# Kernel optimization log

Hardware: AMD Instinct MI355X
Metric: run time of the kernel (lower is better)

Reference implementation:

```python
import jax, jax.numpy as jnp
import numpy as np

N = 1024      # nodes per graph sample
B = 64        # batch size
D_IN = 64     # input feature dim
UNITS = 64    # num_units
K = 2         # max_diffusion_step
NUM_MATRICES = 2 * K + 1


def _random_walk_T(adj):
    # calculate_random_walk_matrix(adj).T == (D^-1 A)^T
    d = adj.sum(axis=1)
    d_inv = jnp.where(d > 0, 1.0 / d, 0.0)
    return (d_inv[:, None] * adj).T


def setup_inputs() -> dict:
    key = jax.random.key(0)
    k1, k2, k3, k4, k5, k6 = jax.random.split(key, 6)
    inputs = jax.random.normal(k1, (B * N, D_IN), dtype=jnp.float32)
    hx = jax.random.normal(k2, (B * N, UNITS), dtype=jnp.float32)
    # sparse-ish weighted adjacency -> random walk Laplacians (transposed) as in Gconv
    adj = jax.random.uniform(k3, (N, N), dtype=jnp.float32)
    adj = adj * (adj > 0.97)
    L0 = _random_walk_T(adj)
    L1 = _random_walk_T(adj.T)
    fan_in = (D_IN + UNITS) * NUM_MATRICES  # 640
    # xavier-normal-ish init
    W1 = jax.random.normal(k4, (fan_in, 2 * UNITS), dtype=jnp.float32) * np.sqrt(2.0 / (fan_in + 2 * UNITS))
    b1 = jnp.zeros((2 * UNITS,), dtype=jnp.float32)
    W2 = jax.random.normal(k5, (fan_in, UNITS), dtype=jnp.float32) * np.sqrt(2.0 / (fan_in + UNITS))
    b2 = jnp.zeros((UNITS,), dtype=jnp.float32)
    return {"inputs": inputs, "hx": hx, "L0": L0, "L1": L1,
            "W1": W1, "b1": b1, "W2": W2, "b2": b2, "batch_size": B}


def _gconv(x_flat, L0, L1, W, b, batch_size):
    # x_flat: [B*N, F]. Chebyshev-style diffusion with two directed random-walk
    # operators (block-diagonal sparse.mm in the original == per-sample matmul).
    n = L0.shape[0]
    f = x_flat.shape[-1]
    x = x_flat.reshape(batch_size, n, f)            # [B, N, F]
    x0a, x0b = x, x
    x1a = jnp.einsum('mn,bnf->bmf', L0, x0a)
    x1b = jnp.einsum('mn,bnf->bmf', L1, x0b)
    outs = [x, x1a, x1b]
    for _ in range(2, K + 1):
        x2a = 2.0 * jnp.einsum('mn,bnf->bmf', L0, x1a) - x0a
        x2b = 2.0 * jnp.einsum('mn,bnf->bmf', L1, x1b) - x0b
        outs += [x2a, x2b]
        x1a, x0a = x2a, x1a
        x1b, x0b = x2b, x1b
    xk = jnp.stack(outs, axis=-1)                   # [B, N, F, num_matrices]
    xk = xk.reshape(batch_size * n, f * NUM_MATRICES)
    return xk @ W + b


def reference(inputs, hx, L0, L1, W1, b1, W2, b2, batch_size):
    # DCGRUCell.forward
    xin = jnp.concatenate([inputs, hx], axis=-1)          # [B*N, D_IN+UNITS]
    value = jax.nn.sigmoid(_gconv(xin, L0, L1, W1, b1, batch_size))
    r, u = jnp.split(value, 2, axis=-1)                   # each [B*N, UNITS]
    xin2 = jnp.concatenate([inputs, r * hx], axis=-1)
    c = jnp.tanh(_gconv(xin2, L0, L1, W2, b2, batch_size))
    new_state = u * hx + (1.0 - u) * c
    return new_state
```

## Files before the change

kernel.cpp:

```cpp
#include <hip/hip_runtime.h>
#include <math.h>

#define N_NODES 1024
#define BATCH   64
#define F_IN    128
#define UNITS   64
#define NUM_M   5
#define CAP     192
#define NT1     640
#define NT2     320
#define DSTR    12

typedef __attribute__((ext_vector_type(8))) short short8v;
typedef __attribute__((ext_vector_type(4))) float f32x4;

__device__ __forceinline__ unsigned short bf16_rne(float x) {
    unsigned u = __float_as_uint(x);
    return (unsigned short)((u + 0x7FFFu + ((u >> 16) & 1u)) >> 16);
}

__global__ void degree_count(const float* __restrict__ L, int* __restrict__ dcnt) {
    int row  = blockIdx.x * 4 + (threadIdx.x >> 6);
    int lane = threadIdx.x & 63;
    const float* Lr = L + (size_t)row * N_NODES;
    int c = 0;
    for (int seg = lane; seg < N_NODES; seg += 64) c += (Lr[seg] != 0.0f);
    #pragma unroll
    for (int o = 1; o < 64; o <<= 1) c += __shfl_xor(c, o);
    if (lane == 0) dcnt[row] = c;
}

__global__ void sort_perm(const int* __restrict__ dcnt, int* __restrict__ perm) {
    __shared__ int hist[CAP + 1];
    __shared__ int offs[CAP + 1];
    int tid = threadIdx.x;
    for (int i = tid; i <= CAP; i += 256) hist[i] = 0;
    __syncthreads();
    for (int r = tid; r < N_NODES; r += 256) {
        int c = dcnt[r]; if (c > CAP) c = CAP;
        atomicAdd(&hist[c], 1);
    }
    __syncthreads();
    if (tid == 0) {
        int s = 0;
        for (int c = CAP; c >= 0; --c) { offs[c] = s; s += hist[c]; }
    }
    __syncthreads();
    for (int r = tid; r < N_NODES; r += 256) {
        int c = dcnt[r]; if (c > CAP) c = CAP;
        int pos = atomicAdd(&offs[c], 1);
        perm[pos] = r;
    }
}

__global__ void ell_build(const float* __restrict__ L, const int* __restrict__ perm,
                          int* __restrict__ scnt, float2* __restrict__ ell) {
    int p    = blockIdx.x * 4 + (threadIdx.x >> 6);
    int lane = threadIdx.x & 63;
    int row  = perm[p];
    const float* Lr = L + (size_t)row * N_NODES;
    int base = 0;
    for (int seg = 0; seg < N_NODES; seg += 64) {
        float v = Lr[seg + lane];
        bool nz = (v != 0.0f);
        unsigned long long bal = __ballot(nz);
        int off = __popcll(bal & ((1ull << lane) - 1ull));
        if (nz) {
            int idx = base + off;
            if (idx < CAP) ell[(size_t)idx * N_NODES + p] =
                               make_float2(__int_as_float(seg + lane), v);
        }
        base += __popcll(bal);
    }
    if (base > CAP) base = CAP;
    for (int idx = base + lane; idx < CAP; idx += 64)
        ell[(size_t)idx * N_NODES + p] = make_float2(__int_as_float(0), 0.0f);
    if (lane == 0) scnt[p] = (base + 3) & ~3;
}

__global__ void wprep_frag(const float* __restrict__ W, unsigned short* __restrict__ Wh,
                           unsigned short* __restrict__ Wl, int nout, int ntot) {
    int idx = blockIdx.x * blockDim.x + threadIdx.x;
    if (idx >= F_IN * ntot) return;
    int jg = idx % ntot, k = idx / ntot;
    int m = jg / nout, j = jg % nout;
    const float* Wk = W + (size_t)(k * NUM_M) * nout;
    float v;
    if (m == 0)      v = Wk[0 * nout + j] - Wk[3 * nout + j] - Wk[4 * nout + j];
    else if (m == 3) v = 2.0f * Wk[3 * nout + j];
    else if (m == 4) v = 2.0f * Wk[4 * nout + j];
    else             v = Wk[(size_t)m * nout + j];
    unsigned short h = bf16_rne(v);
    float hf = __uint_as_float((unsigned)h << 16);
    unsigned short lo = bf16_rne(v - hf);
    size_t fi = ((((size_t)(jg >> 4) * 4 + (k >> 5)) * 64) + ((k >> 3) & 3) * 16 + (jg & 15)) * 8 + (k & 7);
    Wh[fi] = h; Wl[fi] = lo;
}

template <int NCG, int RMUL>
__global__ __launch_bounds__(128, 3) void gemm_proj(
        const float* __restrict__ inp, const float* __restrict__ hx,
        const float* __restrict__ rh,
        const unsigned short* __restrict__ Wh, const unsigned short* __restrict__ Wl,
        float* __restrict__ P, int nrows, int row0) {
    const int tid = threadIdx.x;
    const int lane = tid & 63, w = tid >> 6;
    const int l15 = lane & 15, l4 = lane >> 4;
    const int nbase = blockIdx.x * 64 + w * 32;

    short8v ah[2][4], al[2][4];
    #pragma unroll
    for (int i = 0; i < 2; ++i)
        #pragma unroll
        for (int s = 0; s < 4; ++s) {
            int row_l = nbase + i * 16 + l15;
            int kg8 = s * 4 + l4;
            size_t g = (size_t)(row0 + row_l);
            float x[8];
            if (kg8 < 8) {
                *(float4*)&x[0] = *(const float4*)(inp + g * 64 + kg8 * 8);
                *(float4*)&x[4] = *(const float4*)(inp + g * 64 + kg8 * 8 + 4);
            } else if (RMUL) {
                const float* rp = rh + ((size_t)(kg8 - 8) * nrows + row_l) * 8;
                *(float4*)&x[0] = *(const float4*)(rp);
                *(float4*)&x[4] = *(const float4*)(rp + 4);
            } else {
                *(float4*)&x[0] = *(const float4*)(hx + g * 64 + (kg8 - 8) * 8);
                *(float4*)&x[4] = *(const float4*)(hx + g * 64 + (kg8 - 8) * 8 + 4);
            }
            #pragma unroll
            for (int e = 0; e < 8; ++e) {
                unsigned short h = bf16_rne(x[e]);
                ah[i][s][e] = (short)h;
                al[i][s][e] = (short)bf16_rne(x[e] - __uint_as_float((unsigned)h << 16));
            }
        }

    const int trow = l4 >> 1, toff = (l4 & 1) * 4;
    #pragma unroll 1
    for (int cg = 0; cg < NCG; ++cg) {
        f32x4 acc[2];
        acc[0] = (f32x4){0.f, 0.f, 0.f, 0.f};
        acc[1] = (f32x4){0.f, 0.f, 0.f, 0.f};
        #pragma unroll
        for (int s = 0; s < 4; ++s) {
            size_t o = (((size_t)cg * 4 + s) * 64 + lane) * 8;
            short8v bh = *(const short8v*)(Wh + o);
            short8v bl = *(const short8v*)(Wl + o);
            #pragma unroll
            for (int i = 0; i < 2; ++i) {
                acc[i] = __builtin_amdgcn_mfma_f32_16x16x32_bf16(bh, al[i][s], acc[i], 0, 0, 0);
                acc[i] = __builtin_amdgcn_mfma_f32_16x16x32_bf16(bl, ah[i][s], acc[i], 0, 0, 0);
                acc[i] = __builtin_amdgcn_mfma_f32_16x16x32_bf16(bh, ah[i][s], acc[i], 0, 0, 0);
            }
        }
        #pragma unroll
        for (int i = 0; i < 2; ++i) {
            float4 v = make_float4(acc[i][0], acc[i][1], acc[i][2], acc[i][3]);
            *(float4*)(P + ((size_t)(cg * 2 + trow) * nrows + (nbase + i * 16 + l15)) * 8 + toff) = v;
        }
    }
}

__device__ __forceinline__ void gather2x4(
        const float2* __restrict__ ell, const float* __restrict__ ldsX,
        int tid, int nmax, float4 acc[4][2]) {
    #pragma unroll
    for (int k = 0; k < 4; ++k) {
        acc[k][0] = make_float4(0.f, 0.f, 0.f, 0.f);
        acc[k][1] = make_float4(0.f, 0.f, 0.f, 0.f);
    }
    for (int j = 0; j < nmax; j += 2) {
        const float* e0 = (const float*)(ell + (size_t)j * N_NODES) + (size_t)tid * 8;
        const float* e1 = (const float*)(ell + (size_t)(j + 1) * N_NODES) + (size_t)tid * 8;
        float4 q00 = *(const float4*)e0, q01 = *(const float4*)(e0 + 4);
        float4 q10 = *(const float4*)e1, q11 = *(const float4*)(e1 + 4);
        float cf[2][4], wv[2][4];
        cf[0][0] = q00.x; wv[0][0] = q00.y; cf[0][1] = q00.z; wv[0][1] = q00.w;
        cf[0][2] = q01.x; wv[0][2] = q01.y; cf[0][3] = q01.z; wv[0][3] = q01.w;
        cf[1][0] = q10.x; wv[1][0] = q10.y; cf[1][1] = q10.z; wv[1][1] = q10.w;
        cf[1][2] = q11.x; wv[1][2] = q11.y; cf[1][3] = q11.z; wv[1][3] = q11.w;
        #pragma unroll
        for (int u = 0; u < 2; ++u)
            #pragma unroll
            for (int k = 0; k < 4; ++k) {
                int c = __float_as_int(cf[u][k]);
                float w = wv[u][k];
                const float* xp = ldsX + (size_t)c * DSTR;
                float4 x0 = *(const float4*)xp;
                float4 x1 = *(const float4*)(xp + 4);
                acc[k][0].x += w * x0.x; acc[k][0].y += w * x0.y;
                acc[k][0].z += w * x0.z; acc[k][0].w += w * x0.w;
                acc[k][1].x += w * x1.x; acc[k][1].y += w * x1.y;
                acc[k][1].z += w * x1.z; acc[k][1].w += w * x1.w;
            }
    }
}

__global__ __launch_bounds__(256, 3) void diffuse2(
        const int* __restrict__ scnt0, const float2* __restrict__ ell0, const int* __restrict__ perm0,
        const int* __restrict__ scnt1, const float2* __restrict__ ell1, const int* __restrict__ perm1,
        float* __restrict__ P, size_t sl, int nrows) {
    __shared__ float ldsX[N_NODES * DSTR];
    const int tid = threadIdx.x;
    const int z = blockIdx.z;
    const int*    scnt = z ? scnt1 : scnt0;
    const float2* ell  = z ? ell1  : ell0;
    const int*    perm = z ? perm1 : perm0;
    const float*  src  = P + (size_t)(z ? 4 : 3) * sl;
    float*        dst  = P + (size_t)(z ? 2 : 1) * sl;
    const size_t base = ((size_t)blockIdx.x * nrows + (size_t)blockIdx.y * N_NODES) * 8;

    for (int v = tid; v < 2048; v += 256) {
        float4 d = *(const float4*)(src + base + v * 4);
        *(float4*)(ldsX + (v >> 1) * DSTR + (v & 1) * 4) = d;
    }
    int4 pr = *(const int4*)(perm + tid * 4);
    int4 cn = *(const int4*)(scnt + tid * 4);
    int orow[4] = {pr.x, pr.y, pr.z, pr.w};
    int nn4 = max(max(cn.x, cn.y), max(cn.z, cn.w));
    __syncthreads();

    float4 T[4][2];
    gather2x4(ell, ldsX, tid, nn4, T);
    __syncthreads();
    #pragma unroll
    for (int k = 0; k < 4; ++k) {
        const float* ap = dst + base + (size_t)orow[k] * 8;
        float4 a0 = *(const float4*)ap, a1 = *(const float4*)(ap + 4);
        T[k][0].x += a0.x; T[k][0].y += a0.y; T[k][0].z += a0.z; T[k][0].w += a0.w;
        T[k][1].x += a1.x; T[k][1].y += a1.y; T[k][1].z += a1.z; T[k][1].w += a1.w;
        *(float4*)(ldsX + (size_t)orow[k] * DSTR)     = T[k][0];
        *(float4*)(ldsX + (size_t)orow[k] * DSTR + 4) = T[k][1];
    }
    __syncthreads();
    float4 S[4][2];
    gather2x4(ell, ldsX, tid, nn4, S);
    __syncthreads();
    #pragma unroll
    for (int k = 0; k < 4; ++k) {
        *(float4*)(ldsX + (size_t)orow[k] * DSTR)     = S[k][0];
        *(float4*)(ldsX + (size_t)orow[k] * DSTR + 4) = S[k][1];
    }
    __syncthreads();
    for (int v = tid; v < 2048; v += 256)
        *(float4*)(dst + base + v * 4) = *(const float4*)(ldsX + (v >> 1) * DSTR + (v & 1) * 4);
}

__global__ void combine1(const float* __restrict__ P, const float* __restrict__ b1,
                         const float* __restrict__ hx,
                         float* __restrict__ O1u, float* __restrict__ O1r,
                         int nrows, int row0) {
    int i  = blockIdx.x * 256 + threadIdx.x;
    int ft = blockIdx.y;
    size_t sl = (size_t)16 * nrows * 8;
    size_t o  = ((size_t)ft * nrows + i) * 8;
    float z[8];
    #pragma unroll
    for (int q = 0; q < 8; q += 4) {
        float4 p0 = *(const float4*)(P + o + q);
        float4 p1 = *(const float4*)(P + sl + o + q);
        float4 p2 = *(const float4*)(P + 2 * sl + o + q);
        float4 bb = *(const float4*)(b1 + ft * 8 + q);
        z[q + 0] = 1.f / (1.f + expf(-(p0.x + p1.x + p2.x + bb.x)));
        z[q + 1] = 1.f / (1.f + expf(-(p0.y + p1.y + p2.y + bb.y)));
        z[q + 2] = 1.f / (1.f + expf(-(p0.z + p1.z + p2.z + bb.z)));
        z[q + 3] = 1.f / (1.f + expf(-(p0.w + p1.w + p2.w + bb.w)));
    }
    if (ft >= 8) {
        size_t ou = ((size_t)(ft - 8) * nrows + i) * 8;
        *(float4*)(O1u + ou)     = make_float4(z[0], z[1], z[2], z[3]);
        *(float4*)(O1u + ou + 4) = make_float4(z[4], z[5], z[6], z[7]);
    } else {
        size_t g = (size_t)(row0 + i) * 64 + ft * 8;
        float4 h0 = *(const float4*)(hx + g), h1 = *(const float4*)(hx + g + 4);
        size_t orr = ((size_t)ft * nrows + i) * 8;
        *(float4*)(O1r + orr)     = make_float4(z[0] * h0.x, z[1] * h0.y, z[2] * h0.z, z[3] * h0.w);
        *(float4*)(O1r + orr + 4) = make_float4(z[4] * h1.x, z[5] * h1.y, z[6] * h1.z, z[7] * h1.w);
    }
}

__global__ void combine2(const float* __restrict__ P, const float* __restrict__ b2,
                         const float* __restrict__ O1u, const float* __restrict__ hx,
                         float* __restrict__ out, int nrows, int row0) {
    int i  = blockIdx.x * 256 + threadIdx.x;
    int ft = blockIdx.y;
    size_t sl = (size_t)8 * nrows * 8;
    size_t o  = ((size_t)ft * nrows + i) * 8;
    size_t ou = ((size_t)ft * nrows + i) * 8;
    size_t g  = (size_t)(row0 + i) * 64 + ft * 8;
    #pragma unroll
    for (int q = 0; q < 8; q += 4) {
        float4 p0 = *(const float4*)(P + o + q);
        float4 p1 = *(const float4*)(P + sl + o + q);
        float4 p2 = *(const float4*)(P + 2 * sl + o + q);
        float4 bb = *(const float4*)(b2 + ft * 8 + q);
        float4 u  = *(const float4*)(O1u + ou + q);
        float4 h  = *(const float4*)(hx + g + q);
        float4 r;
        float c;
        c = tanhf(p0.x + p1.x + p2.x + bb.x); r.x = u.x * h.x + (1.f - u.x) * c;
        c = tanhf(p0.y + p1.y + p2.y + bb.y); r.y = u.y * h.y + (1.f - u.y) * c;
        c = tanhf(p0.z + p1.z + p2.z + bb.z); r.z = u.z * h.z + (1.f - u.z) * c;
        c = tanhf(p0.w + p1.w + p2.w + bb.w); r.w = u.w * h.w + (1.f - u.w) * c;
        *(float4*)(out + g + q) = r;
    }
}

extern "C" void kernel_launch(void* const* d_in, const int* in_sizes, int n_in,
                              void* d_out, int out_size, void* d_ws, size_t ws_size,
                              hipStream_t stream) {
    const float* inp = (const float*)d_in[0];
    const float* hx  = (const float*)d_in[1];
    const float* L0  = (const float*)d_in[2];
    const float* L1  = (const float*)d_in[3];
    const float* W1  = (const float*)d_in[4];
    const float* b1  = (const float*)d_in[5];
    const float* W2  = (const float*)d_in[6];
    const float* b2  = (const float*)d_in[7];
    float* out = (float*)d_out;

    char* ws = (char*)d_ws;
    size_t off = 0;
    auto carve = [&](size_t bytes) -> char* {
        off = (off + 255) & ~(size_t)255;
        char* p = ws + off;
        off += bytes;
        return p;
    };
    int*    dcnt  = (int*)   carve(N_NODES * sizeof(int));
    int*    perm0 = (int*)   carve(N_NODES * sizeof(int));
    int*    perm1 = (int*)   carve(N_NODES * sizeof(int));
    int*    scnt0 = (int*)   carve(N_NODES * sizeof(int));
    int*    scnt1 = (int*)   carve(N_NODES * sizeof(int));
    float2* ell0  = (float2*)carve((size_t)N_NODES * CAP * sizeof(float2));
    float2* ell1  = (float2*)carve((size_t)N_NODES * CAP * sizeof(float2));
    unsigned short* Wh1 = (unsigned short*)carve((size_t)F_IN * NT1 * 2);
    unsigned short* Wl1 = (unsigned short*)carve((size_t)F_IN * NT1 * 2);
    unsigned short* Wh2 = (unsigned short*)carve((size_t)F_IN * NT2 * 2);
    unsigned short* Wl2 = (unsigned short*)carve((size_t)F_IN * NT2 * 2);

    size_t per_batch = (size_t)N_NODES * (NT1 + 64 + 64 + NT2) * sizeof(float);
    size_t fixed_end = (off + 255) & ~(size_t)255;
    size_t avail = (ws_size > fixed_end + 4096) ? (ws_size - fixed_end - 4096) : per_batch;
    int maxb = (int)(avail / per_batch);
    int Bc = 1;
    while (Bc * 2 <= maxb && Bc * 2 <= BATCH) Bc *= 2;

    float* Pg1  = (float*)carve((size_t)Bc * N_NODES * NT1 * sizeof(float));
    float* O1u  = (float*)carve((size_t)Bc * N_NODES * 64 * sizeof(float));
    float* O1r  = (float*)carve((size_t)Bc * N_NODES * 64 * sizeof(float));
    float* Pg2  = (float*)carve((size_t)Bc * N_NODES * NT2 * sizeof(float));

    degree_count<<<N_NODES / 4, 256, 0, stream>>>(L0, dcnt);
    sort_perm<<<1, 256, 0, stream>>>(dcnt, perm0);
    ell_build<<<N_NODES / 4, 256, 0, stream>>>(L0, perm0, scnt0, ell0);
    degree_count<<<N_NODES / 4, 256, 0, stream>>>(L1, dcnt);
    sort_perm<<<1, 256, 0, stream>>>(dcnt, perm1);
    ell_build<<<N_NODES / 4, 256, 0, stream>>>(L1, perm1, scnt1, ell1);
    wprep_frag<<<(F_IN * NT1 + 255) / 256, 256, 0, stream>>>(W1, Wh1, Wl1, 128, NT1);
    wprep_frag<<<(F_IN * NT2 + 255) / 256, 256, 0, stream>>>(W2, Wh2, Wl2, 64, NT2);

    for (int b0 = 0; b0 < BATCH; b0 += Bc) {
        int bc = (BATCH - b0 < Bc) ? (BATCH - b0) : Bc;
        int nrows = bc * N_NODES;
        int row0 = b0 * N_NODES;

        gemm_proj<NT1 / 16, 0><<<nrows / 64, 128, 0, stream>>>(
            inp, hx, nullptr, Wh1, Wl1, Pg1, nrows, row0);
        size_t sl1 = (size_t)16 * nrows * 8;
        diffuse2<<<dim3(16, bc, 2), 256, 0, stream>>>(scnt0, ell0, perm0,
            scnt1, ell1, perm1, Pg1, sl1, nrows);
        combine1<<<dim3(nrows / 256, 16), 256, 0, stream>>>(
            Pg1, b1, hx, O1u, O1r, nrows, row0);

        gemm_proj<NT2 / 16, 1><<<nrows / 64, 128, 0, stream>>>(
            inp, hx, O1r, Wh2, Wl2, Pg2, nrows, row0);
        size_t sl2 = (size_t)8 * nrows * 8;
        diffuse2<<<dim3(8, bc, 2), 256, 0, stream>>>(scnt0, ell0, perm0,
            scnt1, ell1, perm1, Pg2, sl2, nrows);
        combine2<<<dim3(nrows / 256, 8), 256, 0, stream>>>(
            Pg2, b2, O1u, hx, out, nrows, row0);
    }
}
```

Measured before the change: 408.0 us.

## Use one thread per node in diffusion kernel with 1024-thread blocks

The diffusion kernel now launches 1024 threads per block, each handling a single graph node, where before 256 threads each handled four nodes. The ELL gather loop is unrolled by four neighbours and reads one float2 entry per slot instead of packed pairs of four-node entries. The intent is more memory-level parallelism and more warps to hide LDS and global latency. The cost is fewer blocks resident per CU given the LDS tile, and the padded ELL loop must be safe to read in steps of four.

```diff
diff --git a/kernel.cpp b/kernel.cpp
--- a/kernel.cpp
+++ b/kernel.cpp
@@ -162,42 +162,36 @@
     }
 }
 
-__device__ __forceinline__ void gather2x4(
+__device__ __forceinline__ void gather1(
         const float2* __restrict__ ell, const float* __restrict__ ldsX,
-        int tid, int nmax, float4 acc[4][2]) {
-    #pragma unroll
-    for (int k = 0; k < 4; ++k) {
-        acc[k][0] = make_float4(0.f, 0.f, 0.f, 0.f);
-        acc[k][1] = make_float4(0.f, 0.f, 0.f, 0.f);
-    }
-    for (int j = 0; j < nmax; j += 2) {
-        const float* e0 = (const float*)(ell + (size_t)j * N_NODES) + (size_t)tid * 8;
-        const float* e1 = (const float*)(ell + (size_t)(j + 1) * N_NODES) + (size_t)tid * 8;
-        float4 q00 = *(const float4*)e0, q01 = *(const float4*)(e0 + 4);
-        float4 q10 = *(const float4*)e1, q11 = *(const float4*)(e1 + 4);
-        float cf[2][4], wv[2][4];
-        cf[0][0] = q00.x; wv[0][0] = q00.y; cf[0][1] = q00.z; wv[0][1] = q00.w;
-        cf[0][2] = q01.x; wv[0][2] = q01.y; cf[0][3] = q01.z; wv[0][3] = q01.w;
-        cf[1][0] = q10.x; wv[1][0] = q10.y; cf[1][1] = q10.z; wv[1][1] = q10.w;
-        cf[1][2] = q11.x; wv[1][2] = q11.y; cf[1][3] = q11.z; wv[1][3] = q11.w;
-        #pragma unroll
-        for (int u = 0; u < 2; ++u)
-            #pragma unroll
-            for (int k = 0; k < 4; ++k) {
-                int c = __float_as_int(cf[u][k]);
-                float w = wv[u][k];
-                const float* xp = ldsX + (size_t)c * DSTR;
-                float4 x0 = *(const float4*)xp;
-                float4 x1 = *(const float4*)(xp + 4);
-                acc[k][0].x += w * x0.x; acc[k][0].y += w * x0.y;
-                acc[k][0].z += w * x0.z; acc[k][0].w += w * x0.w;
-                acc[k][1].x += w * x1.x; acc[k][1].y += w * x1.y;
-                acc[k][1].z += w * x1.z; acc[k][1].w += w * x1.w;
-            }
-    }
-}
-
-__global__ __launch_bounds__(256, 3) void diffuse2(
+        int p, int nn, float4& r0, float4& r1) {
+    r0 = make_float4(0.f, 0.f, 0.f, 0.f);
+    r1 = make_float4(0.f, 0.f, 0.f, 0.f);
+    for (int j = 0; j < nn; j += 4) {
+        float2 e0 = ell[(size_t)(j + 0) * N_NODES + p];
+        float2 e1 = ell[(size_t)(j + 1) * N_NODES + p];
+        float2 e2 = ell[(size_t)(j + 2) * N_NODES + p];
+        float2 e3 = ell[(size_t)(j + 3) * N_NODES + p];
+        const float* x0 = ldsX + (size_t)__float_as_int(e0.x) * DSTR;
+        const float* x1 = ldsX + (size_t)__float_as_int(e1.x) * DSTR;
+        const float* x2 = ldsX + (size_t)__float_as_int(e2.x) * DSTR;
+        const float* x3 = ldsX + (size_t)__float_as_int(e3.x) * DSTR;
+        float4 a0 = *(const float4*)x0, b0 = *(const float4*)(x0 + 4);
+        float4 a1 = *(const float4*)x1, b1 = *(const float4*)(x1 + 4);
+        float4 a2 = *(const float4*)x2, b2 = *(const float4*)(x2 + 4);
+        float4 a3 = *(const float4*)x3, b3 = *(const float4*)(x3 + 4);
+        r0.x += e0.y * a0.x; r0.y += e0.y * a0.y; r0.z += e0.y * a0.z; r0.w += e0.y * a0.w;
+        r1.x += e0.y * b0.x; r1.y += e0.y * b0.y; r1.z += e0.y * b0.z; r1.w += e0.y * b0.w;
+        r0.x += e1.y * a1.x; r0.y += e1.y * a1.y; r0.z += e1.y * a1.z; r0.w += e1.y * a1.w;
+        r1.x += e1.y * b1.x; r1.y += e1.y * b1.y; r1.z += e1.y * b1.z; r1.w += e1.y * b1.w;
+        r0.x += e2.y * a2.x; r0.y += e2.y * a2.y; r0.z += e2.y * a2.z; r0.w += e2.y * a2.w;
+        r1.x += e2.y * b2.x; r1.y += e2.y * b2.y; r1.z += e2.y * b2.z; r1.w += e2.y * b2.w;
+        r0.x += e3.y * a3.x; r0.y += e3.y * a3.y; r0.z += e3.y * a3.z; r0.w += e3.y * a3.w;
+        r1.x += e3.y * b3.x; r1.y += e3.y * b3.y; r1.z += e3.y * b3.z; r1.w += e3.y * b3.w;
+    }
+}
+
+__global__ __launch_bounds__(1024, 2) void diffuse2(
         const int* __restrict__ scnt0, const float2* __restrict__ ell0, const int* __restrict__ perm0,
         const int* __restrict__ scnt1, const float2* __restrict__ ell1, const int* __restrict__ perm1,
         float* __restrict__ P, size_t sl, int nrows) {
@@ -211,39 +205,31 @@
     float*        dst  = P + (size_t)(z ? 2 : 1) * sl;
     const size_t base = ((size_t)blockIdx.x * nrows + (size_t)blockIdx.y * N_NODES) * 8;
 
-    for (int v = tid; v < 2048; v += 256) {
+    for (int v = tid; v < 2048; v += 1024) {
         float4 d = *(const float4*)(src + base + v * 4);
         *(float4*)(ldsX + (v >> 1) * DSTR + (v & 1) * 4) = d;
     }
-    int4 pr = *(const int4*)(perm + tid * 4);
-    int4 cn = *(const int4*)(scnt + tid * 4);
-    int orow[4] = {pr.x, pr.y, pr.z, pr.w};
-    int nn4 = max(max(cn.x, cn.y), max(cn.z, cn.w));
-    __syncthreads();
-
-    float4 T[4][2];
-    gather2x4(ell, ldsX, tid, nn4, T);
-    __syncthreads();
-    #pragma unroll
-    for (int k = 0; k < 4; ++k) {
-        const float* ap = dst + base + (size_t)orow[k] * 8;
-        float4 a0 = *(const float4*)ap, a1 = *(const float4*)(ap + 4);
-        T[k][0].x += a0.x; T[k][0].y += a0.y; T[k][0].z += a0.z; T[k][0].w += a0.w;
-        T[k][1].x += a1.x; T[k][1].y += a1.y; T[k][1].z += a1.z; T[k][1].w += a1.w;
-        *(float4*)(ldsX + (size_t)orow[k] * DSTR)     = T[k][0];
-        *(float4*)(ldsX + (size_t)orow[k] * DSTR + 4) = T[k][1];
-    }
-    __syncthreads();
-    float4 S[4][2];
-    gather2x4(ell, ldsX, tid, nn4, S);
-    __syncthreads();
-    #pragma unroll
-    for (int k = 0; k < 4; ++k) {
-        *(float4*)(ldsX + (size_t)orow[k] * DSTR)     = S[k][0];
-        *(float4*)(ldsX + (size_t)orow[k] * DSTR + 4) = S[k][1];
-    }
-    __syncthreads();
-    for (int v = tid; v < 2048; v += 256)
+    const int orow = perm[tid];
+    const int nn   = scnt[tid];
+    const float* ap = dst + base + (size_t)orow * 8;
+    float4 add0 = *(const float4*)ap, add1 = *(const float4*)(ap + 4);
+    __syncthreads();
+
+    float4 t0, t1;
+    gather1(ell, ldsX, tid, nn, t0, t1);
+    __syncthreads();
+    t0.x += add0.x; t0.y += add0.y; t0.z += add0.z; t0.w += add0.w;
+    t1.x += add1.x; t1.y += add1.y; t1.z += add1.z; t1.w += add1.w;
+    *(float4*)(ldsX + (size_t)orow * DSTR)     = t0;
+    *(float4*)(ldsX + (size_t)orow * DSTR + 4) = t1;
+    __syncthreads();
+    float4 s0, s1;
+    gather1(ell, ldsX, tid, nn, s0, s1);
+    __syncthreads();
+    *(float4*)(ldsX + (size_t)orow * DSTR)     = s0;
+    *(float4*)(ldsX + (size_t)orow * DSTR + 4) = s1;
+    __syncthreads();
+    for (int v = tid; v < 2048; v += 1024)
         *(float4*)(dst + base + v * 4) = *(const float4*)(ldsX + (v >> 1) * DSTR + (v & 1) * 4);
 }
 
@@ -369,7 +355,7 @@
         gemm_proj<NT1 / 16, 0><<<nrows / 64, 128, 0, stream>>>(
             inp, hx, nullptr, Wh1, Wl1, Pg1, nrows, row0);
         size_t sl1 = (size_t)16 * nrows * 8;
-        diffuse2<<<dim3(16, bc, 2), 256, 0, stream>>>(scnt0, ell0, perm0,
+        diffuse2<<<dim3(16, bc, 2), 1024, 0, stream>>>(scnt0, ell0, perm0,
             scnt1, ell1, perm1, Pg1, sl1, nrows);
         combine1<<<dim3(nrows / 256, 16), 256, 0, stream>>>(
             Pg1, b1, hx, O1u, O1r, nrows, row0);
@@ -377,7 +363,7 @@
         gemm_proj<NT2 / 16, 1><<<nrows / 64, 128, 0, stream>>>(
             inp, hx, O1r, Wh2, Wl2, Pg2, nrows, row0);
         size_t sl2 = (size_t)8 * nrows * 8;
-        diffuse2<<<dim3(8, bc, 2), 256, 0, stream>>>(scnt0, ell0, perm0,
+        diffuse2<<<dim3(8, bc, 2), 1024, 0, stream>>>(scnt0, ell0, perm0,
             scnt1, ell1, perm1, Pg2, sl2, nrows);
         combine2<<<dim3(nrows / 256, 8), 256, 0, stream>>>(
             Pg2, b2, O1u, hx, out, nrows, row0);
```

After: 414.2 us. Within noise of the previous version (+1.5%).

## Batch graph preprocessing launches, alias projection buffers, loop feature tiles in diffuse

Applied to the files above, without the earlier changes.

The separate degree-count, sort and ELL-build launches for the two Laplacians are merged into single launches that use a grid dimension to pick the operator, which cuts six preprocessing launches to three. The Pg2 buffer now aliases into Pg1's workspace, so a larger batch chunk Bc fits and the outer loop runs fewer iterations. diffuse2 gains a loop over several feature tiles per block, which caps the grid at about 512 blocks and reuses the perm/scnt loads across tiles. The cost is that each block does serial work across tiles, with extra barriers and less parallelism when chunks are large.

```diff
diff --git a/kernel.cpp b/kernel.cpp
--- a/kernel.cpp
+++ b/kernel.cpp
@@ -19,7 +19,9 @@
     return (unsigned short)((u + 0x7FFFu + ((u >> 16) & 1u)) >> 16);
 }
 
-__global__ void degree_count(const float* __restrict__ L, int* __restrict__ dcnt) {
+__global__ void degree_count(const float* __restrict__ L0, const float* __restrict__ L1,
+                             int* __restrict__ dcnt2) {
+    const float* L = blockIdx.y ? L1 : L0;
     int row  = blockIdx.x * 4 + (threadIdx.x >> 6);
     int lane = threadIdx.x & 63;
     const float* Lr = L + (size_t)row * N_NODES;
@@ -27,12 +29,14 @@
     for (int seg = lane; seg < N_NODES; seg += 64) c += (Lr[seg] != 0.0f);
     #pragma unroll
     for (int o = 1; o < 64; o <<= 1) c += __shfl_xor(c, o);
-    if (lane == 0) dcnt[row] = c;
-}
-
-__global__ void sort_perm(const int* __restrict__ dcnt, int* __restrict__ perm) {
+    if (lane == 0) dcnt2[blockIdx.y * N_NODES + row] = c;
+}
+
+__global__ void sort_perm(const int* __restrict__ dcnt2, int* __restrict__ perm2) {
     __shared__ int hist[CAP + 1];
     __shared__ int offs[CAP + 1];
+    const int* dcnt = dcnt2 + blockIdx.x * N_NODES;
+    int*       perm = perm2 + blockIdx.x * N_NODES;
     int tid = threadIdx.x;
     for (int i = tid; i <= CAP; i += 256) hist[i] = 0;
     __syncthreads();
@@ -53,11 +57,16 @@
     }
 }
 
-__global__ void ell_build(const float* __restrict__ L, const int* __restrict__ perm,
-                          int* __restrict__ scnt, float2* __restrict__ ell) {
+__global__ void ell_build(const float* __restrict__ L0, const float* __restrict__ L1,
+                          const int* __restrict__ perm2,
+                          int* __restrict__ scnt2, float2* __restrict__ ell2) {
+    const int z = blockIdx.y;
+    const float* L = z ? L1 : L0;
+    int* scnt = scnt2 + z * N_NODES;
+    float2* ell = ell2 + (size_t)z * N_NODES * CAP;
     int p    = blockIdx.x * 4 + (threadIdx.x >> 6);
     int lane = threadIdx.x & 63;
-    int row  = perm[p];
+    int row  = perm2[z * N_NODES + p];
     const float* Lr = L + (size_t)row * N_NODES;
     int base = 0;
     for (int seg = 0; seg < N_NODES; seg += 64) {
@@ -198,53 +207,59 @@
 }
 
 __global__ __launch_bounds__(256, 3) void diffuse2(
-        const int* __restrict__ scnt0, const float2* __restrict__ ell0, const int* __restrict__ perm0,
-        const int* __restrict__ scnt1, const float2* __restrict__ ell1, const int* __restrict__ perm1,
-        float* __restrict__ P, size_t sl, int nrows) {
+        const int* __restrict__ scnt2, const float2* __restrict__ ell2,
+        const int* __restrict__ perm2,
+        float* __restrict__ P, size_t sl, int nrows, int ntpb) {
     __shared__ float ldsX[N_NODES * DSTR];
     const int tid = threadIdx.x;
     const int z = blockIdx.z;
-    const int*    scnt = z ? scnt1 : scnt0;
-    const float2* ell  = z ? ell1  : ell0;
-    const int*    perm = z ? perm1 : perm0;
+    const int*    scnt = scnt2 + z * N_NODES;
+    const float2* ell  = ell2 + (size_t)z * N_NODES * CAP;
+    const int*    perm = perm2 + z * N_NODES;
     const float*  src  = P + (size_t)(z ? 4 : 3) * sl;
     float*        dst  = P + (size_t)(z ? 2 : 1) * sl;
-    const size_t base = ((size_t)blockIdx.x * nrows + (size_t)blockIdx.y * N_NODES) * 8;
-
-    for (int v = tid; v < 2048; v += 256) {
-        float4 d = *(const float4*)(src + base + v * 4);
-        *(float4*)(ldsX + (v >> 1) * DSTR + (v & 1) * 4) = d;
-    }
+
     int4 pr = *(const int4*)(perm + tid * 4);
     int4 cn = *(const int4*)(scnt + tid * 4);
     int orow[4] = {pr.x, pr.y, pr.z, pr.w};
     int nn4 = max(max(cn.x, cn.y), max(cn.z, cn.w));
-    __syncthreads();
-
-    float4 T[4][2];
-    gather2x4(ell, ldsX, tid, nn4, T);
-    __syncthreads();
-    #pragma unroll
-    for (int k = 0; k < 4; ++k) {
-        const float* ap = dst + base + (size_t)orow[k] * 8;
-        float4 a0 = *(const float4*)ap, a1 = *(const float4*)(ap + 4);
-        T[k][0].x += a0.x; T[k][0].y += a0.y; T[k][0].z += a0.z; T[k][0].w += a0.w;
-        T[k][1].x += a1.x; T[k][1].y += a1.y; T[k][1].z += a1.z; T[k][1].w += a1.w;
-        *(float4*)(ldsX + (size_t)orow[k] * DSTR)     = T[k][0];
-        *(float4*)(ldsX + (size_t)orow[k] * DSTR + 4) = T[k][1];
-    }
-    __syncthreads();
-    float4 S[4][2];
-    gather2x4(ell, ldsX, tid, nn4, S);
-    __syncthreads();
-    #pragma unroll
-    for (int k = 0; k < 4; ++k) {
-        *(float4*)(ldsX + (size_t)orow[k] * DSTR)     = S[k][0];
-        *(float4*)(ldsX + (size_t)orow[k] * DSTR + 4) = S[k][1];
-    }
-    __syncthreads();
-    for (int v = tid; v < 2048; v += 256)
-        *(float4*)(dst + base + v * 4) = *(const float4*)(ldsX + (v >> 1) * DSTR + (v & 1) * 4);
+
+    #pragma unroll 1
+    for (int t = 0; t < ntpb; ++t) {
+        const int ft = blockIdx.x * ntpb + t;
+        const size_t base = ((size_t)ft * nrows + (size_t)blockIdx.y * N_NODES) * 8;
+        if (t) __syncthreads();
+        for (int v = tid; v < 2048; v += 256) {
+            float4 d = *(const float4*)(src + base + v * 4);
+            *(float4*)(ldsX + (v >> 1) * DSTR + (v & 1) * 4) = d;
+        }
+        __syncthreads();
+
+        float4 T[4][2];
+        gather2x4(ell, ldsX, tid, nn4, T);
+        __syncthreads();
+        #pragma unroll
+        for (int k = 0; k < 4; ++k) {
+            const float* ap = dst + base + (size_t)orow[k] * 8;
+            float4 a0 = *(const float4*)ap, a1 = *(const float4*)(ap + 4);
+            T[k][0].x += a0.x; T[k][0].y += a0.y; T[k][0].z += a0.z; T[k][0].w += a0.w;
+            T[k][1].x += a1.x; T[k][1].y += a1.y; T[k][1].z += a1.z; T[k][1].w += a1.w;
+            *(float4*)(ldsX + (size_t)orow[k] * DSTR)     = T[k][0];
+            *(float4*)(ldsX + (size_t)orow[k] * DSTR + 4) = T[k][1];
+        }
+        __syncthreads();
+        float4 S[4][2];
+        gather2x4(ell, ldsX, tid, nn4, S);
+        __syncthreads();
+        #pragma unroll
+        for (int k = 0; k < 4; ++k) {
+            *(float4*)(ldsX + (size_t)orow[k] * DSTR)     = S[k][0];
+            *(float4*)(ldsX + (size_t)orow[k] * DSTR + 4) = S[k][1];
+        }
+        __syncthreads();
+        for (int v = tid; v < 2048; v += 256)
+            *(float4*)(dst + base + v * 4) = *(const float4*)(ldsX + (v >> 1) * DSTR + (v & 1) * 4);
+    }
 }
 
 __global__ void combine1(const float* __restrict__ P, const float* __restrict__ b1,
@@ -328,36 +343,29 @@
         off += bytes;
         return p;
     };
-    int*    dcnt  = (int*)   carve(N_NODES * sizeof(int));
-    int*    perm0 = (int*)   carve(N_NODES * sizeof(int));
-    int*    perm1 = (int*)   carve(N_NODES * sizeof(int));
-    int*    scnt0 = (int*)   carve(N_NODES * sizeof(int));
-    int*    scnt1 = (int*)   carve(N_NODES * sizeof(int));
-    float2* ell0  = (float2*)carve((size_t)N_NODES * CAP * sizeof(float2));
-    float2* ell1  = (float2*)carve((size_t)N_NODES * CAP * sizeof(float2));
+    int*    dcnt2 = (int*)   carve(2 * N_NODES * sizeof(int));
+    int*    perm2 = (int*)   carve(2 * N_NODES * sizeof(int));
+    int*    scnt2 = (int*)   carve(2 * N_NODES * sizeof(int));
+    float2* ell2  = (float2*)carve((size_t)2 * N_NODES * CAP * sizeof(float2));
     unsigned short* Wh1 = (unsigned short*)carve((size_t)F_IN * NT1 * 2);
     unsigned short* Wl1 = (unsigned short*)carve((size_t)F_IN * NT1 * 2);
     unsigned short* Wh2 = (unsigned short*)carve((size_t)F_IN * NT2 * 2);
     unsigned short* Wl2 = (unsigned short*)carve((size_t)F_IN * NT2 * 2);
 
-    size_t per_batch = (size_t)N_NODES * (NT1 + 64 + 64 + NT2) * sizeof(float);
+    size_t per_batch = (size_t)N_NODES * (88 * 8 + 64 + 64) * sizeof(float);
     size_t fixed_end = (off + 255) & ~(size_t)255;
     size_t avail = (ws_size > fixed_end + 4096) ? (ws_size - fixed_end - 4096) : per_batch;
     int maxb = (int)(avail / per_batch);
     int Bc = 1;
     while (Bc * 2 <= maxb && Bc * 2 <= BATCH) Bc *= 2;
 
-    float* Pg1  = (float*)carve((size_t)Bc * N_NODES * NT1 * sizeof(float));
+    float* Pg1  = (float*)carve((size_t)Bc * N_NODES * 88 * 8 * sizeof(float));
     float* O1u  = (float*)carve((size_t)Bc * N_NODES * 64 * sizeof(float));
     float* O1r  = (float*)carve((size_t)Bc * N_NODES * 64 * sizeof(float));
-    float* Pg2  = (float*)carve((size_t)Bc * N_NODES * NT2 * sizeof(float));
-
-    degree_count<<<N_NODES / 4, 256, 0, stream>>>(L0, dcnt);
-    sort_perm<<<1, 256, 0, stream>>>(dcnt, perm0);
-    ell_build<<<N_NODES / 4, 256, 0, stream>>>(L0, perm0, scnt0, ell0);
-    degree_count<<<N_NODES / 4, 256, 0, stream>>>(L1, dcnt);
-    sort_perm<<<1, 256, 0, stream>>>(dcnt, perm1);
-    ell_build<<<N_NODES / 4, 256, 0, stream>>>(L1, perm1, scnt1, ell1);
+
+    degree_count<<<dim3(N_NODES / 4, 2), 256, 0, stream>>>(L0, L1, dcnt2);
+    sort_perm<<<2, 256, 0, stream>>>(dcnt2, perm2);
+    ell_build<<<dim3(N_NODES / 4, 2), 256, 0, stream>>>(L0, L1, perm2, scnt2, ell2);
     wprep_frag<<<(F_IN * NT1 + 255) / 256, 256, 0, stream>>>(W1, Wh1, Wl1, 128, NT1);
     wprep_frag<<<(F_IN * NT2 + 255) / 256, 256, 0, stream>>>(W2, Wh2, Wl2, 64, NT2);
 
@@ -365,20 +373,24 @@
         int bc = (BATCH - b0 < Bc) ? (BATCH - b0) : Bc;
         int nrows = bc * N_NODES;
         int row0 = b0 * N_NODES;
+        float* Pg2 = Pg1 + (size_t)48 * nrows * 8;
+
+        int ntpb1 = 1; while ((16 / ntpb1) * bc * 2 > 512 && ntpb1 < 16) ntpb1 *= 2;
+        int ntpb2 = 1; while ((8  / ntpb2) * bc * 2 > 512 && ntpb2 < 8)  ntpb2 *= 2;
 
         gemm_proj<NT1 / 16, 0><<<nrows / 64, 128, 0, stream>>>(
             inp, hx, nullptr, Wh1, Wl1, Pg1, nrows, row0);
         size_t sl1 = (size_t)16 * nrows * 8;
-        diffuse2<<<dim3(16, bc, 2), 256, 0, stream>>>(scnt0, ell0, perm0,
-            scnt1, ell1, perm1, Pg1, sl1, nrows);
+        diffuse2<<<dim3(16 / ntpb1, bc, 2), 256, 0, stream>>>(
+            scnt2, ell2, perm2, Pg1, sl1, nrows, ntpb1);
         combine1<<<dim3(nrows / 256, 16), 256, 0, stream>>>(
             Pg1, b1, hx, O1u, O1r, nrows, row0);
 
         gemm_proj<NT2 / 16, 1><<<nrows / 64, 128, 0, stream>>>(
             inp, hx, O1r, Wh2, Wl2, Pg2, nrows, row0);
         size_t sl2 = (size_t)8 * nrows * 8;
-        diffuse2<<<dim3(8, bc, 2), 256, 0, stream>>>(scnt0, ell0, perm0,
-            scnt1, ell1, perm1, Pg2, sl2, nrows);
+        diffuse2<<<dim3(8 / ntpb2, bc, 2), 256, 0, stream>>>(
+            scnt2, ell2, perm2, Pg2, sl2, nrows, ntpb2);
         combine2<<<dim3(nrows / 256, 8), 256, 0, stream>>>(
             Pg2, b2, O1u, hx, out, nrows, row0);
     }
```

New measurement: 346.0 us. 15.2% less time.
